# Kernel optimization log

Measured on AMD Instinct MI355X. Metric: run time of the kernel, lower is better.

The kernel has to match this reference:

```python
import jax, jax.numpy as jnp
import numpy as np

BETA = 0.25


def setup_inputs() -> dict:
    key = jax.random.key(0)
    k1, k2 = jax.random.split(key)
    z = jax.random.normal(k1, (8, 256, 16, 16, 16), dtype=jnp.float32)
    n_codes, dim = 2048, 256
    # original init: uniform(-1/n_codes, 1/n_codes)
    emb = jax.random.uniform(k2, (n_codes, dim), dtype=jnp.float32,
                             minval=-1.0 / n_codes, maxval=1.0 / n_codes)
    return {"z": z, "emb": emb}


def reference(z, emb):
    B, C, D, H, W = z.shape  # C == embedding_dim
    # channels-last flatten: [B*D*H*W, C]
    z_flat = jnp.transpose(z, (0, 2, 3, 4, 1)).reshape(-1, C)
    # squared L2 distances to each code: [N, K]
    dist = (jnp.sum(z_flat * z_flat, axis=1, keepdims=True)
            + jnp.sum(emb * emb, axis=1)
            - 2.0 * jnp.dot(z_flat, emb.T))
    idx = jnp.argmin(dist, axis=1)  # [N] int
    # FAITHFUL to original: gathered codes are reshaped directly to z.shape
    # (B, C, D, H, W) WITHOUT undoing the channels-last permute.
    z_q = jnp.take(emb, idx, axis=0).reshape(z.shape)
    commitment_loss = jnp.mean((jax.lax.stop_gradient(z_q) - z) ** 2)
    codebook_loss = jnp.mean((z_q - jax.lax.stop_gradient(z)) ** 2)
    vq_loss = codebook_loss + BETA * commitment_loss
    z_q_st = z + jax.lax.stop_gradient(z_q - z)  # straight-through
    return (z_q_st, vq_loss, idx)
```

## Files before the change

### kernel.cpp

```cpp
#include <hip/hip_runtime.h>
#include <float.h>

#define N_PTS    32768
#define N_CODES  2048
#define DIM      256
#define S_STRIDE 4096
#define B_STRIDE 1048576
#define N_ELEM   8388608

#define MARGIN   8e-4f

#define WS_PARTIAL 0
#define WS_E2      512
#define WS_EB      8704
#define WS_ZT      1057280
#define WS_TMIN    17834496
#define WS_EMBP    WS_ZT

typedef unsigned short ushort_t;
typedef short bf16x8 __attribute__((ext_vector_type(8)));
typedef float f32x4 __attribute__((ext_vector_type(4)));

__device__ __forceinline__ ushort_t f2bf(float v) {
    const unsigned u = __float_as_uint(v);
    return (ushort_t)((u + 0x7FFFu + ((u >> 16) & 1u)) >> 16);
}

__device__ __forceinline__ void async_copy16(void* lds, const void* g) {
    __builtin_amdgcn_global_load_lds(
        (const __attribute__((address_space(1))) unsigned int*)g,
        (__attribute__((address_space(3))) unsigned int*)lds, 16, 0, 0);
}

__device__ __forceinline__ void nt_store4(float* p, f32x4 v) {
    __builtin_nontemporal_store(v, reinterpret_cast<f32x4*>(p));
}

__global__ void conv_emb_kernel(const float* __restrict__ emb, ushort_t* __restrict__ eb) {
    const int gid = blockIdx.x * 256 + threadIdx.x;
    const int k = gid >> 6, c4 = gid & 63;
    const float4 u = *reinterpret_cast<const float4*>(emb + (size_t)k * DIM + c4 * 4);
    ushort4 v; v.x = f2bf(u.x); v.y = f2bf(u.y); v.z = f2bf(u.z); v.w = f2bf(u.w);
    *reinterpret_cast<ushort4*>(eb + (size_t)k * DIM + c4 * 4) = v;
}

__global__ void perm_emb_kernel(const float* __restrict__ emb, float* __restrict__ embp) {
    const int gid = blockIdx.x * 256 + threadIdx.x;
    const int ql = gid & 15, c4 = (gid >> 4) & 63, g = gid >> 10;
    const float4 u = reinterpret_cast<const float4*>(emb)[(size_t)(g * 16 + ql) * 64 + c4];
    reinterpret_cast<float4*>(embp)[gid] = u;
}

__global__ void e2p_kernel(const float* __restrict__ emb, float* __restrict__ e2,
                           float* __restrict__ partial) {
    const int k = blockIdx.x * 256 + threadIdx.x;
    if (blockIdx.x == 0 && threadIdx.x < 64) partial[threadIdx.x] = 0.f;
    const float* base = emb + (size_t)k * DIM;
    float half[2];
    #pragma unroll
    for (int h = 0; h < 2; ++h) {
        float r[8];
        #pragma unroll
        for (int j = 0; j < 8; ++j) { const float v = base[h * 128 + j]; r[j] = __fmul_rn(v, v); }
        for (int t = 8; t < 128; t += 8)
            #pragma unroll
            for (int j = 0; j < 8; ++j) {
                const float v = base[h * 128 + t + j];
                r[j] = __fadd_rn(r[j], __fmul_rn(v, v));
            }
        half[h] = __fadd_rn(__fadd_rn(__fadd_rn(r[0], r[1]), __fadd_rn(r[2], r[3])),
                            __fadd_rn(__fadd_rn(r[4], r[5]), __fadd_rn(r[6], r[7])));
    }
    e2[k] = __fadd_rn(half[0], half[1]);
}

__global__ void transpose_kernel(const float* __restrict__ z, ushort_t* __restrict__ zt) {
    __shared__ ushort_t lt[64][72];
    const int bx = blockIdx.x;
    const int b = bx >> 8, cg = (bx >> 6) & 3, sg = bx & 63;
    const int c0 = cg * 64, s0 = sg * 64;
    const int t = threadIdx.x;
    {
        const int cl = t >> 4, s4 = t & 15;
        #pragma unroll
        for (int j = 0; j < 4; ++j) {
            const int c = cl + 16 * j;
            const float4 u = *reinterpret_cast<const float4*>(
                z + (size_t)b * B_STRIDE + (size_t)(c0 + c) * S_STRIDE + s0 + s4 * 4);
            ushort4 v; v.x = f2bf(u.x); v.y = f2bf(u.y); v.z = f2bf(u.z); v.w = f2bf(u.w);
            *reinterpret_cast<ushort4*>(&lt[c][s4 * 4]) = v;
        }
    }
    __syncthreads();
    {
        const int sl = t >> 4, c4 = t & 15;
        #pragma unroll
        for (int j = 0; j < 4; ++j) {
            const int s = sl + 16 * j;
            ushort4 v;
            v.x = lt[c4 * 4 + 0][s]; v.y = lt[c4 * 4 + 1][s];
            v.z = lt[c4 * 4 + 2][s]; v.w = lt[c4 * 4 + 3][s];
            *reinterpret_cast<ushort4*>(zt + (size_t)(b * 4096 + s0 + s) * DIM + c0 + c4 * 4) = v;
        }
    }
}

__global__ __launch_bounds__(256, 4) void screen_kernel(
    const ushort_t* __restrict__ zt, const ushort_t* __restrict__ eb,
    const float* __restrict__ e2, float* __restrict__ tmin)
{
    __shared__ char lds[32768];
    __shared__ float e2s[128];
    const int tid = threadIdx.x;
    const int x = blockIdx.x;
    const int bm = (x & 7) * 32 + ((x >> 3) & 31), bn = x >> 8;
    const int n0 = bm * 128, k0 = bn * 128;
    if (tid < 128) e2s[tid] = e2[k0 + tid];
    const int wv = tid >> 6, lane = tid & 63;
    const int col = lane & 15, quad = lane >> 4;
    const int pcr = quad ^ ((col >> 1) & 3);

    f32x4 acc[2][8];
    #pragma unroll
    for (int j = 0; j < 2; ++j)
        #pragma unroll
        for (int i = 0; i < 8; ++i) acc[j][i] = (f32x4){0.f, 0.f, 0.f, 0.f};

    #define STAGE(kc_, half_)                                                       \
        {                                                                           \
            const int base_ = (half_) * 16384;                                      \
            _Pragma("unroll")                                                       \
            for (int it = 0; it < 4; ++it) {                                        \
                const int L = tid + it * 256;                                       \
                if (L < 512) {                                                      \
                    const int row = L >> 2, pc = L & 3, c = pc ^ ((row >> 1) & 3);  \
                    async_copy16(lds + base_ + L * 16,                              \
                                 zt + ((size_t)(n0 + row) * DIM + (kc_) * 32 + c * 8)); \
                } else {                                                            \
                    const int L2 = L - 512;                                         \
                    const int row = L2 >> 2, pc = L2 & 3, c = pc ^ ((row >> 1) & 3);\
                    async_copy16(lds + base_ + 8192 + L2 * 16,                      \
                                 eb + ((size_t)(k0 + row) * DIM + (kc_) * 32 + c * 8)); \
                }                                                                   \
            }                                                                       \
        }

    STAGE(0, 0);
    __syncthreads();
    #pragma unroll
    for (int kc = 0; kc < 8; ++kc) {
        const int cur = kc & 1;
        if (kc < 7) STAGE(kc + 1, cur ^ 1);
        {
            const char* zb = lds + cur * 16384;
            const char* ebb = zb + 8192;
            bf16x8 af[2];
            #pragma unroll
            for (int j = 0; j < 2; ++j) {
                const int crow = wv * 32 + j * 16 + col;
                af[j] = *reinterpret_cast<const bf16x8*>(ebb + (crow * 4 + pcr) * 16);
            }
            #pragma unroll
            for (int i = 0; i < 8; ++i) {
                const int prow = i * 16 + col;
                const bf16x8 bq = *reinterpret_cast<const bf16x8*>(zb + (prow * 4 + pcr) * 16);
                #pragma unroll
                for (int j = 0; j < 2; ++j)
                    acc[j][i] = __builtin_amdgcn_mfma_f32_16x16x32_bf16(af[j], bq, acc[j][i], 0, 0, 0);
            }
        }
        __syncthreads();
    }
    #undef STAGE

    float* res = reinterpret_cast<float*>(lds);
    float ej[2][4];
    #pragma unroll
    for (int j = 0; j < 2; ++j) {
        const f32x4 e4 = *reinterpret_cast<const f32x4*>(&e2s[wv * 32 + j * 16 + quad * 4]);
        ej[j][0] = e4[0]; ej[j][1] = e4[1]; ej[j][2] = e4[2]; ej[j][3] = e4[3];
    }
    #pragma unroll
    for (int j = 0; j < 2; ++j) {
        #pragma unroll
        for (int i = 0; i < 8; ++i) {
            float tm[4];
            #pragma unroll
            for (int r = 0; r < 4; ++r) tm[r] = fmaf(-2.f, acc[j][i][r], ej[j][r]);
            float m = fminf(fminf(tm[0], tm[1]), fminf(tm[2], tm[3]));
            m = fminf(m, __shfl_xor(m, 16));
            m = fminf(m, __shfl_xor(m, 32));
            if (quad == 0)
                res[(i * 16 + col) * 12 + wv * 2 + j] = m;
        }
    }
    __syncthreads();
    {
        const int p = tid >> 1, h = tid & 1;
        const f32x4 v = *reinterpret_cast<const f32x4*>(&res[p * 12 + h * 4]);
        *reinterpret_cast<f32x4*>(
            &tmin[((size_t)bn * N_PTS + n0 + p) * 8 + h * 4]) = v;
    }
}

__global__ __launch_bounds__(256, 3) void exact_kernel(
    const float* __restrict__ z, const float* __restrict__ emb,
    const float* __restrict__ embp,
    const float* __restrict__ e2, const float* __restrict__ tmin,
    float* __restrict__ outf, float* __restrict__ out_idx, float* __restrict__ partial)
{
    __shared__ float zs[32 * 260];
    const int tid = threadIdx.x;
    const int n0 = blockIdx.x * 32;
    const int b = n0 >> 12, s0 = n0 & 4095;
    {
        const int tq = tid & 7, cg = tid >> 3;
        for (int c = cg; c < DIM; c += 32) {
            const float4 u = *reinterpret_cast<const float4*>(
                z + (size_t)b * B_STRIDE + (size_t)c * S_STRIDE + s0 + tq * 4);
            zs[(tq * 4 + 0) * 260 + c] = u.x;
            zs[(tq * 4 + 1) * 260 + c] = u.y;
            zs[(tq * 4 + 2) * 260 + c] = u.z;
            zs[(tq * 4 + 3) * 260 + c] = u.w;
        }
    }
    __syncthreads();
    const int wv = tid >> 6, lane = tid & 63;
    const int quad = lane >> 4, ql = lane & 15;
    float lossacc = 0.f;

    float a[2][8];
    #pragma unroll
    for (int t = 0; t < 2; ++t) {
        const int n = n0 + wv * 8 + t * 4 + quad;
        #pragma unroll
        for (int i = 0; i < 8; ++i)
            a[t][i] = __builtin_nontemporal_load(
                tmin + ((size_t)(i * 2 + (ql >> 3)) * N_PTS + n) * 8 + (ql & 7));
    }

    #pragma unroll
    for (int t = 0; t < 2; ++t) {
        const int p = wv * 8 + t * 4 + quad;
        const int n = n0 + p;
        const float* zr = &zs[p * 260];
        const int h = ql >> 3, j = ql & 7;
        float v0 = zr[h * 128 + j];
        float r = __fmul_rn(v0, v0);
        #pragma unroll
        for (int t2 = 1; t2 < 16; ++t2) {
            const float v = zr[h * 128 + j + 8 * t2];
            r = __fadd_rn(r, __fmul_rn(v, v));
        }
        { float v = __shfl_xor(r, 1); r = __fadd_rn(r, v); }
        { float v = __shfl_xor(r, 2); r = __fadd_rn(r, v); }
        { float v = __shfl_xor(r, 4); r = __fadd_rn(r, v); }
        const float z2n = __fadd_rn(__shfl(r, quad * 16), __shfl(r, quad * 16 + 8));
        float mn = fminf(fminf(fminf(a[t][0], a[t][1]), fminf(a[t][2], a[t][3])),
                         fminf(fminf(a[t][4], a[t][5]), fminf(a[t][6], a[t][7])));
        #pragma unroll
        for (int off = 1; off < 16; off <<= 1) mn = fminf(mn, __shfl_xor(mn, off));
        const float thr = mn + MARGIN;
        unsigned long long M0 = 0ull, M1 = 0ull;
        #pragma unroll
        for (int i = 0; i < 8; ++i) {
            const unsigned long long bal = __ballot(a[t][i] <= thr);
            const unsigned long long bits = (bal >> (quad * 16)) & 0xFFFFull;
            if (i < 4) M0 |= bits << (i * 16);
            else       M1 |= bits << ((i - 4) * 16);
        }
        float bs = FLT_MAX; int bk = 0x7FFFFFFF;
        while (__any((M0 | M1) != 0ull)) {
            int myt = -1;
            if (M0) { myt = __ffsll(M0) - 1; M0 &= M0 - 1; }
            else if (M1) { myt = 64 + __ffsll(M1) - 1; M1 &= M1 - 1; }
            if (myt >= 0) {
                const int kg = myt * 16 + ql;
                const float e2k = e2[kg];
                const float4* gp = reinterpret_cast<const float4*>(embp)
                                   + (size_t)myt * 1024 + ql;
                float4 pre[8];
                #pragma unroll
                for (int s8 = 0; s8 < 8; ++s8) pre[s8] = gp[s8 * 16];
                float dot = 0.f;
                #pragma unroll
                for (int seg = 0; seg < 8; ++seg) {
                    float4 cur[8];
                    #pragma unroll
                    for (int s8 = 0; s8 < 8; ++s8) cur[s8] = pre[s8];
                    if (seg < 7) {
                        #pragma unroll
                        for (int s8 = 0; s8 < 8; ++s8)
                            pre[s8] = gp[(seg + 1) * 128 + s8 * 16];
                    }
                    #pragma unroll
                    for (int s8 = 0; s8 < 8; ++s8) {
                        const int c4 = seg * 8 + s8;
                        const float4 zv = *reinterpret_cast<const float4*>(zr + c4 * 4);
                        dot = fmaf(zv.x, cur[s8].x, dot);
                        dot = fmaf(zv.y, cur[s8].y, dot);
                        dot = fmaf(zv.z, cur[s8].z, dot);
                        dot = fmaf(zv.w, cur[s8].w, dot);
                    }
                }
                const float A = __fadd_rn(z2n, e2k);
                const float s = __fsub_rn(A, __fmul_rn(2.f, dot));
                if (s < bs || (s == bs && kg < bk)) { bs = s; bk = kg; }
            }
        }
        #pragma unroll
        for (int off = 1; off < 16; off <<= 1) {
            const float os = __shfl_xor(bs, off);
            const int ok = __shfl_xor(bk, off);
            if (os < bs || (os == bs && ok < bk)) { bs = os; bk = ok; }
        }
        const float* eq = emb + (size_t)bk * DIM;
        float* op = outf + (size_t)n * DIM;
        #pragma unroll
        for (int jj = 0; jj < 4; ++jj) {
            const int c = (jj * 16 + ql) * 4;
            const float4 q4 = *reinterpret_cast<const float4*>(eq + c);
            f32x4 q; q[0] = q4.x; q[1] = q4.y; q[2] = q4.z; q[3] = q4.w;
            nt_store4(op + c, q);
            float d;
            d = q4.x - zr[c + 0]; lossacc = fmaf(d, d, lossacc);
            d = q4.y - zr[c + 1]; lossacc = fmaf(d, d, lossacc);
            d = q4.z - zr[c + 2]; lossacc = fmaf(d, d, lossacc);
            d = q4.w - zr[c + 3]; lossacc = fmaf(d, d, lossacc);
        }
        if (ql == 0) out_idx[n] = (float)bk;
    }
    #pragma unroll
    for (int off = 1; off < 64; off <<= 1) lossacc += __shfl_xor(lossacc, off);
    if (lane == 0) atomicAdd(&partial[blockIdx.x & 63], lossacc);
}

__global__ void finalize_kernel(const float* __restrict__ partial, float* __restrict__ out_loss) {
    float v = partial[threadIdx.x];
    #pragma unroll
    for (int off = 1; off < 64; off <<= 1) v += __shfl_xor(v, off);
    if (threadIdx.x == 0)
        *out_loss = v * 1.25f / (float)N_ELEM;
}

extern "C" void kernel_launch(void* const* d_in, const int* in_sizes, int n_in,
                              void* d_out, int out_size, void* d_ws, size_t ws_size,
                              hipStream_t stream) {
    const float* z = (const float*)d_in[0];
    const float* emb = (const float*)d_in[1];
    char* ws = (char*)d_ws;
    float* partial = (float*)(ws + WS_PARTIAL);
    float* e2 = (float*)(ws + WS_E2);
    ushort_t* eb = (ushort_t*)(ws + WS_EB);
    ushort_t* zt = (ushort_t*)(ws + WS_ZT);
    float* embp = (float*)(ws + WS_EMBP);
    float* tmin = (float*)(ws + WS_TMIN);
    float* outf = (float*)d_out;
    float* out_loss = outf + N_ELEM;
    float* out_idx = outf + N_ELEM + 1;

    conv_emb_kernel<<<512, 256, 0, stream>>>(emb, eb);
    e2p_kernel<<<N_CODES / 256, 256, 0, stream>>>(emb, e2, partial);
    transpose_kernel<<<2048, 256, 0, stream>>>(z, zt);
    screen_kernel<<<4096, 256, 0, stream>>>(zt, eb, e2, tmin);
    perm_emb_kernel<<<512, 256, 0, stream>>>(emb, embp);
    exact_kernel<<<N_PTS / 32, 256, 0, stream>>>(z, emb, embp, e2, tmin, outf, out_idx, partial);
    finalize_kernel<<<1, 64, 0, stream>>>(partial, out_loss);
}
```

Before: 217.1 us.

## Skip exact fp32 rescoring when bf16 screen top-2 gap exceeds margin

The screen kernel now also records, for each point and each 128-code block, the best code index and the best and second-best approximate distances, and writes them to a new stats buffer. The exact kernel merges these across blocks and, when the gap between the best and runner-up exceeds the margin, takes the screened index directly. It then skips the squared-norm computation and the fp32 candidate rescoring loop for that point. This costs extra epilogue work and stats writes in the screen kernel, and it relies on the bf16 error bound (MARGIN) to keep the argmin exact.

```diff
diff --git a/kernel.cpp b/kernel.cpp
--- a/kernel.cpp
+++ b/kernel.cpp
@@ -15,6 +15,7 @@
 #define WS_EB      8704
 #define WS_ZT      1057280
 #define WS_TMIN    17834496
+#define WS_STATS   34611712
 #define WS_EMBP    WS_ZT
 
 typedef unsigned short ushort_t;
@@ -107,7 +108,8 @@
 
 __global__ __launch_bounds__(256, 4) void screen_kernel(
     const ushort_t* __restrict__ zt, const ushort_t* __restrict__ eb,
-    const float* __restrict__ e2, float* __restrict__ tmin)
+    const float* __restrict__ e2, float* __restrict__ tmin,
+    float* __restrict__ stats)
 {
     __shared__ char lds[32768];
     __shared__ float e2s[128];
@@ -173,7 +175,8 @@
     }
     #undef STAGE
 
-    float* res = reinterpret_cast<float*>(lds);
+    float* res  = reinterpret_cast<float*>(lds);
+    float* sbuf = reinterpret_cast<float*>(lds + 8192);
     float ej[2][4];
     #pragma unroll
     for (int j = 0; j < 2; ++j) {
@@ -194,6 +197,34 @@
                 res[(i * 16 + col) * 12 + wv * 2 + j] = m;
         }
     }
+    #pragma unroll
+    for (int i = 0; i < 8; ++i) {
+        float m1 = FLT_MAX, m2 = FLT_MAX; int i1 = 0;
+        #pragma unroll
+        for (int j = 0; j < 2; ++j) {
+            #pragma unroll
+            for (int r = 0; r < 4; ++r) {
+                const float v = fmaf(-2.f, acc[j][i][r], ej[j][r]);
+                const int idx = k0 + wv * 32 + j * 16 + quad * 4 + r;
+                if (v < m1) { m2 = m1; m1 = v; i1 = idx; }
+                else if (v < m2) { m2 = v; }
+            }
+        }
+        #pragma unroll
+        for (int off = 16; off <= 32; off <<= 1) {
+            const float om1 = __shfl_xor(m1, off);
+            const float om2 = __shfl_xor(m2, off);
+            const int   oi1 = __shfl_xor(i1, off);
+            if (om1 < m1) { m2 = fminf(om2, m1); m1 = om1; i1 = oi1; }
+            else          { m2 = fminf(m2, om1); }
+        }
+        if (quad == 0) {
+            const int p = i * 16 + col;
+            sbuf[p * 12 + wv * 3 + 0] = m1;
+            sbuf[p * 12 + wv * 3 + 1] = (float)i1;
+            sbuf[p * 12 + wv * 3 + 2] = m2;
+        }
+    }
     __syncthreads();
     {
         const int p = tid >> 1, h = tid & 1;
@@ -201,12 +232,27 @@
         *reinterpret_cast<f32x4*>(
             &tmin[((size_t)bn * N_PTS + n0 + p) * 8 + h * 4]) = v;
     }
+    if (tid < 128) {
+        const int p = tid;
+        float m1 = sbuf[p * 12 + 0], i1 = sbuf[p * 12 + 1], m2 = sbuf[p * 12 + 2];
+        #pragma unroll
+        for (int w = 1; w < 4; ++w) {
+            const float bm1 = sbuf[p * 12 + w * 3 + 0];
+            const float bi1 = sbuf[p * 12 + w * 3 + 1];
+            const float bm2 = sbuf[p * 12 + w * 3 + 2];
+            if (bm1 < m1) { m2 = fminf(m1, bm2); m1 = bm1; i1 = bi1; }
+            else          { m2 = fminf(m2, bm1); }
+        }
+        f32x4 st; st[0] = m1; st[1] = i1; st[2] = m2; st[3] = 0.f;
+        *reinterpret_cast<f32x4*>(&stats[((size_t)bn * N_PTS + n0 + p) * 4]) = st;
+    }
 }
 
 __global__ __launch_bounds__(256, 3) void exact_kernel(
     const float* __restrict__ z, const float* __restrict__ emb,
     const float* __restrict__ embp,
     const float* __restrict__ e2, const float* __restrict__ tmin,
+    const float* __restrict__ stats,
     float* __restrict__ outf, float* __restrict__ out_idx, float* __restrict__ partial)
 {
     __shared__ float zs[32 * 260];
@@ -229,7 +275,7 @@
     const int quad = lane >> 4, ql = lane & 15;
     float lossacc = 0.f;
 
-    float a[2][8];
+    float a[2][8]; f32x4 st[2];
     #pragma unroll
     for (int t = 0; t < 2; ++t) {
         const int n = n0 + wv * 8 + t * 4 + quad;
@@ -237,6 +283,7 @@
         for (int i = 0; i < 8; ++i)
             a[t][i] = __builtin_nontemporal_load(
                 tmin + ((size_t)(i * 2 + (ql >> 3)) * N_PTS + n) * 8 + (ql & 7));
+        st[t] = *reinterpret_cast<const f32x4*>(&stats[((size_t)ql * N_PTS + n) * 4]);
     }
 
     #pragma unroll
@@ -244,76 +291,89 @@
         const int p = wv * 8 + t * 4 + quad;
         const int n = n0 + p;
         const float* zr = &zs[p * 260];
-        const int h = ql >> 3, j = ql & 7;
-        float v0 = zr[h * 128 + j];
-        float r = __fmul_rn(v0, v0);
-        #pragma unroll
-        for (int t2 = 1; t2 < 16; ++t2) {
-            const float v = zr[h * 128 + j + 8 * t2];
-            r = __fadd_rn(r, __fmul_rn(v, v));
-        }
-        { float v = __shfl_xor(r, 1); r = __fadd_rn(r, v); }
-        { float v = __shfl_xor(r, 2); r = __fadd_rn(r, v); }
-        { float v = __shfl_xor(r, 4); r = __fadd_rn(r, v); }
-        const float z2n = __fadd_rn(__shfl(r, quad * 16), __shfl(r, quad * 16 + 8));
-        float mn = fminf(fminf(fminf(a[t][0], a[t][1]), fminf(a[t][2], a[t][3])),
-                         fminf(fminf(a[t][4], a[t][5]), fminf(a[t][6], a[t][7])));
-        #pragma unroll
-        for (int off = 1; off < 16; off <<= 1) mn = fminf(mn, __shfl_xor(mn, off));
-        const float thr = mn + MARGIN;
-        unsigned long long M0 = 0ull, M1 = 0ull;
-        #pragma unroll
-        for (int i = 0; i < 8; ++i) {
-            const unsigned long long bal = __ballot(a[t][i] <= thr);
-            const unsigned long long bits = (bal >> (quad * 16)) & 0xFFFFull;
-            if (i < 4) M0 |= bits << (i * 16);
-            else       M1 |= bits << ((i - 4) * 16);
-        }
-        float bs = FLT_MAX; int bk = 0x7FFFFFFF;
-        while (__any((M0 | M1) != 0ull)) {
-            int myt = -1;
-            if (M0) { myt = __ffsll(M0) - 1; M0 &= M0 - 1; }
-            else if (M1) { myt = 64 + __ffsll(M1) - 1; M1 &= M1 - 1; }
-            if (myt >= 0) {
-                const int kg = myt * 16 + ql;
-                const float e2k = e2[kg];
-                const float4* gp = reinterpret_cast<const float4*>(embp)
-                                   + (size_t)myt * 1024 + ql;
-                float4 pre[8];
-                #pragma unroll
-                for (int s8 = 0; s8 < 8; ++s8) pre[s8] = gp[s8 * 16];
-                float dot = 0.f;
-                #pragma unroll
-                for (int seg = 0; seg < 8; ++seg) {
-                    float4 cur[8];
+        float m1 = st[t][0], i1f = st[t][1], m2 = st[t][2];
+        #pragma unroll
+        for (int off = 1; off < 16; off <<= 1) {
+            const float om1 = __shfl_xor(m1, off);
+            const float oi1 = __shfl_xor(i1f, off);
+            const float om2 = __shfl_xor(m2, off);
+            if (om1 < m1) { m2 = fminf(m1, om2); m1 = om1; i1f = oi1; }
+            else          { m2 = fminf(m2, om1); }
+        }
+        const bool shortcut = (m2 - m1 > MARGIN);
+        float bs = FLT_MAX; int bkf = 0x7FFFFFFF;
+        if (!shortcut) {
+            const int h = ql >> 3, j = ql & 7;
+            float v0 = zr[h * 128 + j];
+            float r = __fmul_rn(v0, v0);
+            #pragma unroll
+            for (int t2 = 1; t2 < 16; ++t2) {
+                const float v = zr[h * 128 + j + 8 * t2];
+                r = __fadd_rn(r, __fmul_rn(v, v));
+            }
+            { float v = __shfl_xor(r, 1); r = __fadd_rn(r, v); }
+            { float v = __shfl_xor(r, 2); r = __fadd_rn(r, v); }
+            { float v = __shfl_xor(r, 4); r = __fadd_rn(r, v); }
+            const float z2n = __fadd_rn(__shfl(r, quad * 16), __shfl(r, quad * 16 + 8));
+            float mn = fminf(fminf(fminf(a[t][0], a[t][1]), fminf(a[t][2], a[t][3])),
+                             fminf(fminf(a[t][4], a[t][5]), fminf(a[t][6], a[t][7])));
+            #pragma unroll
+            for (int off = 1; off < 16; off <<= 1) mn = fminf(mn, __shfl_xor(mn, off));
+            const float thr = mn + MARGIN;
+            unsigned long long M0 = 0ull, M1 = 0ull;
+            #pragma unroll
+            for (int i = 0; i < 8; ++i) {
+                const unsigned long long bal = __ballot(a[t][i] <= thr);
+                const unsigned long long bits = (bal >> (quad * 16)) & 0xFFFFull;
+                if (i < 4) M0 |= bits << (i * 16);
+                else       M1 |= bits << ((i - 4) * 16);
+            }
+            while (__any((M0 | M1) != 0ull)) {
+                int myt = -1;
+                if (M0) { myt = __ffsll(M0) - 1; M0 &= M0 - 1; }
+                else if (M1) { myt = 64 + __ffsll(M1) - 1; M1 &= M1 - 1; }
+                if (myt >= 0) {
+                    const int kg = myt * 16 + ql;
+                    const float e2k = e2[kg];
+                    const float4* gp = reinterpret_cast<const float4*>(embp)
+                                       + (size_t)myt * 1024 + ql;
+                    float4 pre[8];
                     #pragma unroll
-                    for (int s8 = 0; s8 < 8; ++s8) cur[s8] = pre[s8];
-                    if (seg < 7) {
+                    for (int s8 = 0; s8 < 8; ++s8) pre[s8] = gp[s8 * 16];
+                    float dot = 0.f;
+                    #pragma unroll
+                    for (int seg = 0; seg < 8; ++seg) {
+                        float4 cur[8];
                         #pragma unroll
-                        for (int s8 = 0; s8 < 8; ++s8)
-                            pre[s8] = gp[(seg + 1) * 128 + s8 * 16];
+                        for (int s8 = 0; s8 < 8; ++s8) cur[s8] = pre[s8];
+                        if (seg < 7) {
+                            #pragma unroll
+                            for (int s8 = 0; s8 < 8; ++s8)
+                                pre[s8] = gp[(seg + 1) * 128 + s8 * 16];
+                        }
+                        #pragma unroll
+                        for (int s8 = 0; s8 < 8; ++s8) {
+                            const int c4 = seg * 8 + s8;
+                            const float4 zv = *reinterpret_cast<const float4*>(zr + c4 * 4);
+                            dot = fmaf(zv.x, cur[s8].x, dot);
+                            dot = fmaf(zv.y, cur[s8].y, dot);
+                            dot = fmaf(zv.z, cur[s8].z, dot);
+                            dot = fmaf(zv.w, cur[s8].w, dot);
+                        }
                     }
-                    #pragma unroll
-                    for (int s8 = 0; s8 < 8; ++s8) {
-                        const int c4 = seg * 8 + s8;
-                        const float4 zv = *reinterpret_cast<const float4*>(zr + c4 * 4);
-                        dot = fmaf(zv.x, cur[s8].x, dot);
-                        dot = fmaf(zv.y, cur[s8].y, dot);
-                        dot = fmaf(zv.z, cur[s8].z, dot);
-                        dot = fmaf(zv.w, cur[s8].w, dot);
-                    }
+                    const float A = __fadd_rn(z2n, e2k);
+                    const float s = __fsub_rn(A, __fmul_rn(2.f, dot));
+                    if (s < bs || (s == bs && kg < bkf)) { bs = s; bkf = kg; }
                 }
-                const float A = __fadd_rn(z2n, e2k);
-                const float s = __fsub_rn(A, __fmul_rn(2.f, dot));
-                if (s < bs || (s == bs && kg < bk)) { bs = s; bk = kg; }
-            }
-        }
-        #pragma unroll
-        for (int off = 1; off < 16; off <<= 1) {
-            const float os = __shfl_xor(bs, off);
-            const int ok = __shfl_xor(bk, off);
-            if (os < bs || (os == bs && ok < bk)) { bs = os; bk = ok; }
-        }
+            }
+            #pragma unroll
+            for (int off = 1; off < 16; off <<= 1) {
+                const float os = __shfl_xor(bs, off);
+                const int ok = __shfl_xor(bkf, off);
+                if (os < bs || (os == bs && ok < bkf)) { bs = os; bkf = ok; }
+            }
+        }
+        const int bk = shortcut ? (int)i1f : bkf;
         const float* eq = emb + (size_t)bk * DIM;
         float* op = outf + (size_t)n * DIM;
         #pragma unroll
@@ -355,6 +415,7 @@
     ushort_t* zt = (ushort_t*)(ws + WS_ZT);
     float* embp = (float*)(ws + WS_EMBP);
     float* tmin = (float*)(ws + WS_TMIN);
+    float* stats = (float*)(ws + WS_STATS);
     float* outf = (float*)d_out;
     float* out_loss = outf + N_ELEM;
     float* out_idx = outf + N_ELEM + 1;
@@ -362,8 +423,9 @@
     conv_emb_kernel<<<512, 256, 0, stream>>>(emb, eb);
     e2p_kernel<<<N_CODES / 256, 256, 0, stream>>>(emb, e2, partial);
     transpose_kernel<<<2048, 256, 0, stream>>>(z, zt);
-    screen_kernel<<<4096, 256, 0, stream>>>(zt, eb, e2, tmin);
+    screen_kernel<<<4096, 256, 0, stream>>>(zt, eb, e2, tmin, stats);
     perm_emb_kernel<<<512, 256, 0, stream>>>(emb, embp);
-    exact_kernel<<<N_PTS / 32, 256, 0, stream>>>(z, emb, embp, e2, tmin, outf, out_idx, partial);
+    exact_kernel<<<N_PTS / 32, 256, 0, stream>>>(z, emb, embp, e2, tmin, stats,
+                                                 outf, out_idx, partial);
     finalize_kernel<<<1, 64, 0, stream>>>(partial, out_loss);
 }
```

New measurement: 232.0 us. 6.9% more time.
